# Kernel tuning notes

Hardware: AMD Instinct MI355X
Metric: run time of the kernel (lower is better)

The kernel has to match this reference:

```python
import jax, jax.numpy as jnp
import numpy as np

N = 50000      # nodes
E = 800000     # edges (avg degree 16)
DIN = 128      # input_dim
DG = 128       # gnn_dim
DCLS = 128     # cls_dim
DOUT = 10      # output_dim
LMDA = 1.0     # rw_lmda
P_DROP = 0.5


def setup_inputs() -> dict:
    key = jax.random.key(0)
    ks = jax.random.split(key, 12)
    x = jax.random.normal(ks[0], (N, DIN), jnp.float32)
    edge_index = jax.random.randint(ks[1], (2, E), 0, N, dtype=jnp.int64)
    edge_weight = jax.random.uniform(ks[2], (E,), jnp.float32)
    def glorot(k, shape):
        lim = np.sqrt(6.0 / (shape[0] + shape[1])).astype(np.float32)
        return jax.random.uniform(k, shape, jnp.float32, -lim, lim)
    return dict(
        x=x, edge_index=edge_index, edge_weight=edge_weight,
        W_lin_in=glorot(ks[3], (DIN, DG)), b_lin_in=jnp.zeros((DG,), jnp.float32),
        W_agg_in=glorot(ks[4], (DG + DIN, DG)), b_agg_in=jnp.zeros((DG,), jnp.float32),
        W_lin_h=glorot(ks[5], (DG, DG)), b_lin_h=jnp.zeros((DG,), jnp.float32),
        W_agg_h=glorot(ks[6], (2 * DG, DG)), b_agg_h=jnp.zeros((DG,), jnp.float32),
        W_mlp1=glorot(ks[7], (DG, DCLS)), b_mlp1=jnp.zeros((DCLS,), jnp.float32),
        W_mlp2=glorot(ks[8], (DCLS, DOUT)), b_mlp2=jnp.zeros((DOUT,), jnp.float32),
    )


def _gs_layer(x, row, col, ew, inv_cnt, W_lin, b_lin, W_agg, b_agg):
    # GS_reweight: message = (1-lmda)*lin(x_j) + lmda*ew*lin(x_j), mean-aggregated
    # at row (flow='target_to_source': gather from col, scatter to row).
    h = x @ W_lin + b_lin                      # [N, DG] (lin before gather == lin(x_j))
    hj = h[col]                                # [E, DG] gather
    m = (1.0 - LMDA) * hj + LMDA * (ew[:, None] * hj)
    agg = jax.ops.segment_sum(m, row, num_segments=N) * inv_cnt[:, None]  # mean
    out = jnp.concatenate([agg, x], axis=-1) @ W_agg + b_agg              # update()
    return jax.nn.relu(out)


def _dropout(x, k):
    mask = jax.random.bernoulli(k, 1.0 - P_DROP, x.shape)
    return jnp.where(mask, x / (1.0 - P_DROP), 0.0)


def reference(x, edge_index, edge_weight,
              W_lin_in, b_lin_in, W_agg_in, b_agg_in,
              W_lin_h, b_lin_h, W_agg_h, b_agg_h,
              W_mlp1, b_mlp1, W_mlp2, b_mlp2):
    row, col = edge_index[0], edge_index[1]
    cnt = jax.ops.segment_sum(jnp.ones((E,), x.dtype), row, num_segments=N)
    inv_cnt = 1.0 / jnp.maximum(cnt, 1.0)     # scatter_mean: empty rows -> 0
    dk = jax.random.split(jax.random.key(42), 3)
    h = _gs_layer(x, row, col, edge_weight, inv_cnt, W_lin_in, b_lin_in, W_agg_in, b_agg_in)
    h = _dropout(jax.nn.relu(h), dk[0])       # relu is idempotent after update's relu
    for i in range(2):                        # layers 2,3 share prop_hidden weights
        h = _gs_layer(h, row, col, edge_weight, inv_cnt, W_lin_h, b_lin_h, W_agg_h, b_agg_h)
        h = _dropout(jax.nn.relu(h), dk[i + 1])
    y = jax.nn.relu(h @ W_mlp1 + b_mlp1) @ W_mlp2 + b_mlp2  # cls_layers=2, bn=False
    return (h, y)
```

## Files before the change

kernel.cpp:

```cpp
#include <hip/hip_runtime.h>
#include <cstdint>
#include <cstddef>


#define N_NODES 50000
#define N_EDGES 800000
#define DGN 128
#define DOUT 10
#define NELEM (N_NODES * DGN)
#define NMASKW (NELEM / 64)
#define NBINS 391
#define TILE 4096
#define BSTR 4096
#define NTILES ((N_EDGES + TILE - 1) / TILE)
#define GB128 ((N_NODES + 127) / 128)
#define MK_BLOCKS 25000
#define MKB512 12500

#define XB_BLK 6250
#define HI_BLK NTILES
#define WC_BLK 128
#define TR_BLK 192
#define R0 XB_BLK
#define R1 (R0 + HI_BLK)
#define R2 (R1 + WC_BLK)
#define R3 (R2 + TR_BLK)
#define MEGA_BLOCKS (R3 + 1)

#define AB_BLOCKS ((N_NODES + 3) / 4)

typedef __attribute__((ext_vector_type(8))) short bf16x8;
typedef __attribute__((ext_vector_type(4))) float f32x4;

__host__ __device__ static inline unsigned short f2bf(float f) {
  union { float f; unsigned u; } c; c.f = f;
  unsigned u = c.u;
  return (unsigned short)((u + 0x7fffu + ((u >> 16) & 1u)) >> 16);
}
__device__ static inline float bflo(unsigned u) { return __uint_as_float(u << 16); }
__device__ static inline float bfhi(unsigned u) { return __uint_as_float(u & 0xffff0000u); }

__host__ __device__ static inline void tf2x32(unsigned k0, unsigned k1,
                                              unsigned c0, unsigned c1,
                                              unsigned& o0, unsigned& o1) {
  unsigned ks2 = k0 ^ k1 ^ 0x1BD11BDAu;
  unsigned x0 = c0 + k0;
  unsigned x1 = c1 + k1;
#define TFR(r) { x0 += x1; x1 = (x1 << (r)) | (x1 >> (32 - (r))); x1 ^= x0; }
  TFR(13) TFR(15) TFR(26) TFR(6)
  x0 += k1;  x1 += ks2 + 1u;
  TFR(17) TFR(29) TFR(16) TFR(24)
  x0 += ks2; x1 += k0 + 2u;
  TFR(13) TFR(15) TFR(26) TFR(6)
  x0 += k0;  x1 += k1 + 3u;
  TFR(17) TFR(29) TFR(16) TFR(24)
  x0 += k1;  x1 += ks2 + 4u;
  TFR(13) TFR(15) TFR(26) TFR(6)
  x0 += ks2; x1 += k0 + 5u;
#undef TFR
  o0 = x0; o1 = x1;
}

__device__ static inline void mask_chunk(unsigned long long* __restrict__ gm,
                                         int i, unsigned k0, unsigned k1) {
  unsigned o0, o1;
  tf2x32(k0, k1, 0u, (unsigned)i, o0, o1);
  unsigned long long b = __ballot(((o0 ^ o1) >> 31) == 0u);
  if ((threadIdx.x & 63) == 0) gm[i >> 6] = b;
}

__global__ __launch_bounds__(256) void mega_kernel(
    const float* __restrict__ x, unsigned short* __restrict__ xb,
    const int* __restrict__ ei, int* __restrict__ chist,
    const float* __restrict__ Wli, const float* __restrict__ Wai,
    const float* __restrict__ Wlh, const float* __restrict__ Wah,
    const float* __restrict__ Wm1,
    const float* __restrict__ bli, const float* __restrict__ blh,
    unsigned short* __restrict__ Tai, unsigned short* __restrict__ Tah,
    unsigned short* __restrict__ Tm1,
    float* __restrict__ bvi, float* __restrict__ bvh) {
  __shared__ int h[NBINS];
  const int b = blockIdx.x;
  const int tid = threadIdx.x;

  if (b < R0) {
    int g = b * 256 + tid;
    float4 v = ((const float4*)x)[g];
    ushort4 o;
    o.x = f2bf(v.x); o.y = f2bf(v.y); o.z = f2bf(v.z); o.w = f2bf(v.w);
    ((ushort4*)xb)[g] = o;
  } else if (b < R1) {
    for (int i = tid; i < NBINS; i += 256) h[i] = 0;
    __syncthreads();
    const int e0 = (b - R0) * TILE;
#pragma unroll 4
    for (int j = 0; j < TILE; j += 256) {
      int e = e0 + j + tid;
      if (e < N_EDGES) {
        int r = ei[e];
        r = (r < 0) ? 0 : (r >= N_NODES ? N_NODES - 1 : r);
        atomicAdd(&h[r >> 7], 1);
      }
    }
    __syncthreads();
    for (int i = tid; i < NBINS; i += 256)
      if (h[i]) atomicAdd(&chist[i], h[i]);
  } else if (b < R2) {
    int idx = (b - R1) * 256 + tid;
    int n = idx & 127;
    int k = (idx >> 7) & 127;
    int m = idx >> 14;
    const float* Wl = m ? Wlh : Wli;
    const float* Wa = m ? Wah : Wai;
    unsigned short* T = m ? Tah : Tai;
    float acc = 0.0f;
#pragma unroll 8
    for (int j = 0; j < 128; ++j)
      acc += Wl[k * 128 + j] * Wa[j * 128 + n];
    T[n * 256 + k] = f2bf(acc);
  } else if (b < R3) {
    int j = (b - R2) * 256 + tid;
    if (j < 16384) {
      int kk = j & 127, n = j >> 7;
      Tai[n * 256 + 128 + kk] = f2bf(Wai[(size_t)(128 + kk) * 128 + n]);
    } else if (j < 32768) {
      int q = j - 16384;
      int kk = q & 127, n = q >> 7;
      Tah[n * 256 + 128 + kk] = f2bf(Wah[(size_t)(128 + kk) * 128 + n]);
    } else {
      int q = j - 32768;
      int k = q & 127, n = q >> 7;
      Tm1[n * 128 + k] = f2bf(Wm1[(size_t)k * 128 + n]);
    }
  } else {
    int n = tid & 127;
    const float* bl = (tid < 128) ? bli : blh;
    const float* Wa = (tid < 128) ? Wai : Wah;
    float acc = 0.0f;
    for (int j = 0; j < 128; ++j) acc += bl[j] * Wa[j * 128 + n];
    if (tid < 128) bvi[n] = acc; else bvh[n] = acc;
  }
}

__global__ __launch_bounds__(256) void scatter_kernel(const int* __restrict__ ei,
                                                      const float* __restrict__ ew,
                                                      int* __restrict__ ccursor,
                                                      uint2* __restrict__ pk,
                                                      unsigned long long* __restrict__ mg0,
                                                      unsigned k00, unsigned k01) {
  if (blockIdx.x >= NTILES) {
    mask_chunk(mg0, (blockIdx.x - NTILES) * 256 + threadIdx.x, k00, k01);
    return;
  }
  __shared__ uint2 st[TILE];
  __shared__ unsigned short sbin[TILE];
  __shared__ int h[NBINS];
  __shared__ int base[NBINS];
  __shared__ int gbase[NBINS];
  __shared__ int cur[NBINS];
  __shared__ int sc[512];
  const int tid = threadIdx.x;
  const int e0 = blockIdx.x * TILE;
  const int nt = (N_EDGES - e0 < TILE) ? (N_EDGES - e0) : TILE;

  for (int i = tid; i < NBINS; i += 256) { h[i] = 0; cur[i] = 0; }
  __syncthreads();
  for (int j = tid; j < nt; j += 256) {
    int r = ei[e0 + j];
    r = (r < 0) ? 0 : (r >= N_NODES ? N_NODES - 1 : r);
    atomicAdd(&h[r >> 7], 1);
  }
  __syncthreads();
  sc[tid] = (tid < NBINS) ? h[tid] : 0;
  sc[tid + 256] = (tid + 256 < NBINS) ? h[tid + 256] : 0;
  __syncthreads();
  for (int off = 1; off < 512; off <<= 1) {
    int a0 = (tid >= off) ? sc[tid - off] : 0;
    int a1 = (tid + 256 >= off) ? sc[tid + 256 - off] : 0;
    __syncthreads();
    sc[tid] += a0; sc[tid + 256] += a1;
    __syncthreads();
  }
  if (tid < NBINS) {
    base[tid] = sc[tid] - h[tid];
    if (h[tid]) gbase[tid] = tid * BSTR + atomicAdd(&ccursor[tid], h[tid]);
  }
  if (tid + 256 < NBINS) {
    base[tid + 256] = sc[tid + 256] - h[tid + 256];
    if (h[tid + 256])
      gbase[tid + 256] = (tid + 256) * BSTR + atomicAdd(&ccursor[tid + 256], h[tid + 256]);
  }
  __syncthreads();
  for (int j = tid; j < nt; j += 256) {
    int r = ei[e0 + j];
    r = (r < 0) ? 0 : (r >= N_NODES ? N_NODES - 1 : r);
    int c = ei[N_EDGES + e0 + j];
    c = (c < 0) ? 0 : (c >= N_NODES ? N_NODES - 1 : c);
    int bb = r >> 7;
    int slot = base[bb] + atomicAdd(&cur[bb], 1);
    uint2 p;
    p.x = ((unsigned)r << 16) | (unsigned)c;
    p.y = __float_as_uint(ew[e0 + j]);
    st[slot] = p;
    sbin[slot] = (unsigned short)bb;
  }
  __syncthreads();
  for (int j = tid; j < nt; j += 256) {
    int bb = sbin[j];
    pk[(size_t)gbase[bb] + (j - base[bb])] = st[j];
  }
}

__global__ __launch_bounds__(256) void place_kernel(const int* __restrict__ chist,
                                                    const uint2* __restrict__ pk,
                                                    uint2* __restrict__ csr,
                                                    int* __restrict__ rowptr,
                                                    float* __restrict__ invc) {
  __shared__ int red[256];
  __shared__ int lcnt[128];
  __shared__ int lpre[128];
  __shared__ int lcur[128];
  __shared__ int sc[128];
  const int b = blockIdx.x;
  const int tid = threadIdx.x;

  int psum = 0;
  for (int i = tid; i < b; i += 256) psum += chist[i];
  red[tid] = psum;
  __syncthreads();
  for (int off = 128; off > 0; off >>= 1) {
    if (tid < off) red[tid] += red[tid + off];
    __syncthreads();
  }
  const int cb = red[0];
  const int n = chist[b];
  const uint2* __restrict__ pkb = pk + (size_t)b * BSTR;
  const int r0 = b << 7;
  const int nr = (N_NODES - r0 < 128) ? (N_NODES - r0) : 128;

  if (tid < 128) { lcnt[tid] = 0; lcur[tid] = 0; }
  __syncthreads();
  for (int i = tid; i < n; i += 256) {
    int r7 = (int)(pkb[i].x >> 16) - r0;
    atomicAdd(&lcnt[r7], 1);
  }
  __syncthreads();
  if (tid < 128) sc[tid] = lcnt[tid];
  __syncthreads();
  for (int off = 1; off < 128; off <<= 1) {
    int tv = (tid >= off && tid < 128) ? sc[tid - off] : 0;
    __syncthreads();
    if (tid < 128) sc[tid] += tv;
    __syncthreads();
  }
  if (tid < 128) lpre[tid] = sc[tid] - lcnt[tid];
  __syncthreads();
  if (tid < nr) {
    rowptr[r0 + tid] = cb + lpre[tid];
    int c = lcnt[tid];
    invc[r0 + tid] = 1.0f / (float)(c > 1 ? c : 1);
  }
  if (b == NBINS - 1 && tid == 0) rowptr[N_NODES] = N_EDGES;
  for (int i = tid; i < n; i += 256) {
    uint2 p = pkb[i];
    int r7 = (int)(p.x >> 16) - r0;
    int slot = cb + lpre[r7] + atomicAdd(&lcur[r7], 1);
    uint2 o;
    o.x = p.x & 0xFFFFu;
    o.y = p.y;
    csr[slot] = o;
  }
}

__global__ __launch_bounds__(256) void agg_kernel(const unsigned short* __restrict__ hlin,
                                                  const int* __restrict__ rowptr,
                                                  const uint2* __restrict__ csr,
                                                  const float* __restrict__ invc,
                                                  unsigned short* __restrict__ agg,
                                                  float* __restrict__ swout) {
  const int r = blockIdx.x * 4 + (threadIdx.x >> 6);
  const int lane = threadIdx.x & 63;
  const int es = lane >> 4;
  const int cg = lane & 15;
  const int start = rowptr[r];
  const int num = rowptr[r + 1] - start;
  const uint4* __restrict__ H = (const uint4*)hlin;

  int qi = (num > 0) ? (start + (lane < num ? lane : num - 1)) : 0;
  uint2 myq = csr[qi];

  float a[8] = {0.f, 0.f, 0.f, 0.f, 0.f, 0.f, 0.f, 0.f};
  float ws = 0.f;
  const int nb = (num < 64) ? num : 64;
  for (int e = 0; e < nb; e += 16) {
#pragma unroll
    for (int j = 0; j < 4; ++j) {
      int idx = e + j * 4 + es;
      bool ok = idx < nb;
      int sl = ok ? idx : nb - 1;
      int c0 = __shfl((int)myq.x, sl);
      int w0 = __shfl((int)myq.y, sl);
      unsigned col = (unsigned)c0;
      float w = ok ? __uint_as_float((unsigned)w0) : 0.0f;
      uint4 p = H[(size_t)col * 16 + cg];
      ws += w;
      a[0] += w * bflo(p.x); a[1] += w * bfhi(p.x);
      a[2] += w * bflo(p.y); a[3] += w * bfhi(p.y);
      a[4] += w * bflo(p.z); a[5] += w * bfhi(p.z);
      a[6] += w * bflo(p.w); a[7] += w * bfhi(p.w);
    }
  }
  for (int e = 64; e < num; e += 16) {
#pragma unroll
    for (int j = 0; j < 4; ++j) {
      int idx = e + j * 4 + es;
      bool ok = idx < num;
      int idxc = ok ? idx : (num - 1);
      uint2 q = csr[start + idxc];
      float w = ok ? __uint_as_float(q.y) : 0.0f;
      uint4 p = H[(size_t)q.x * 16 + cg];
      ws += w;
      a[0] += w * bflo(p.x); a[1] += w * bfhi(p.x);
      a[2] += w * bflo(p.y); a[3] += w * bfhi(p.y);
      a[4] += w * bflo(p.z); a[5] += w * bfhi(p.z);
      a[6] += w * bflo(p.w); a[7] += w * bfhi(p.w);
    }
  }
#pragma unroll
  for (int k = 0; k < 8; ++k) {
    a[k] += __shfl_xor(a[k], 32);
    a[k] += __shfl_xor(a[k], 16);
  }
  ws += __shfl_xor(ws, 32);
  ws += __shfl_xor(ws, 16);
  const float s = invc[r];
  if (es == 0) {
    uint4 o;
    o.x = (unsigned)f2bf(a[0] * s) | ((unsigned)f2bf(a[1] * s) << 16);
    o.y = (unsigned)f2bf(a[2] * s) | ((unsigned)f2bf(a[3] * s) << 16);
    o.z = (unsigned)f2bf(a[4] * s) | ((unsigned)f2bf(a[5] * s) << 16);
    o.w = (unsigned)f2bf(a[6] * s) | ((unsigned)f2bf(a[7] * s) << 16);
    ((uint4*)agg)[(size_t)r * 16 + cg] = o;
  }
  if (swout && lane == 0) swout[r] = ws * s;
}

template <bool WF32, bool MASKGEN, bool MLP>
__global__ __launch_bounds__(512) void layer_gemm(
    const unsigned short* __restrict__ Agg, const unsigned short* __restrict__ Hin,
    const unsigned short* __restrict__ Wt,
    const float* __restrict__ bvec, const float* __restrict__ bagg,
    const float* __restrict__ sw,
    const unsigned long long* __restrict__ maskw,
    float* __restrict__ outf, unsigned short* __restrict__ outb,
    unsigned long long* __restrict__ gm, unsigned gk0, unsigned gk1,
    const unsigned short* __restrict__ Wt2,
    const float* __restrict__ b1,
    const float* __restrict__ W2, const float* __restrict__ b2,
    float* __restrict__ y) {
  if (MASKGEN && blockIdx.x >= GB128) {
    mask_chunk(gm, (blockIdx.x - GB128) * 512 + threadIdx.x, gk0, gk1);
    return;
  }
  constexpr int LS = 72;
  constexpr int LT = 132;
  __shared__ unsigned short Als[128 * LS];
  __shared__ unsigned short Bls[128 * LS];
  __shared__ unsigned short tT[MLP ? 128 * LT : 2];
  __shared__ unsigned short Wsb[MLP ? 16 * LT : 2];
  __shared__ float bs[MLP ? DOUT : 1];
  const int tid = threadIdx.x;
  const int m0 = blockIdx.x * 128;
  const int lane = tid & 63;
  const int wid = tid >> 6;
  const int wm = (wid >> 1) * 32;
  const int wn = (wid & 1) * 64;
  const int ln = lane & 15;
  const int lh = lane >> 4;
  const int sArow = tid >> 2;
  const int sAk = (tid & 3) * 16;
  int arow = m0 + sArow;
  if (arow >= N_NODES) arow = N_NODES - 1;

  if (MLP) {
    for (int i = tid; i < 16 * 128; i += 512) {
      int c = i >> 7, k = i & 127;
      Wsb[c * LT + k] = (c < DOUT) ? f2bf(W2[(size_t)k * DOUT + c]) : (unsigned short)0;
    }
    if (tid < DOUT) bs[tid] = b2[tid];
  }

  f32x4 acc[2][4];
#pragma unroll
  for (int i = 0; i < 2; ++i)
#pragma unroll
    for (int j = 0; j < 4; ++j)
#pragma unroll
      for (int r = 0; r < 4; ++r) acc[i][j][r] = 0.0f;

  for (int kb = 0; kb < 256; kb += 64) {
    const unsigned short* Asrc = (kb < 128) ? Agg : Hin;
    const unsigned short* ap = Asrc + (size_t)arow * 128 + (kb & 127) + sAk;
    unsigned short* al = &Als[sArow * LS + sAk];
    *(uint4*)(al + 0) = *(const uint4*)(ap + 0);
    *(uint4*)(al + 8) = *(const uint4*)(ap + 8);
    const unsigned short* bp = Wt + (size_t)sArow * 256 + kb + sAk;
    unsigned short* bl = &Bls[sArow * LS + sAk];
    *(uint4*)(bl + 0) = *(const uint4*)(bp + 0);
    *(uint4*)(bl + 8) = *(const uint4*)(bp + 8);
    __syncthreads();
#pragma unroll
    for (int ks = 0; ks < 64; ks += 32) {
      bf16x8 af[2], bfr[4];
#pragma unroll
      for (int i = 0; i < 2; ++i)
        af[i] = *(const bf16x8*)&Als[(wm + i * 16 + ln) * LS + ks + lh * 8];
#pragma unroll
      for (int j = 0; j < 4; ++j)
        bfr[j] = *(const bf16x8*)&Bls[(wn + j * 16 + ln) * LS + ks + lh * 8];
#pragma unroll
      for (int i = 0; i < 2; ++i)
#pragma unroll
        for (int j = 0; j < 4; ++j)
          acc[i][j] = __builtin_amdgcn_mfma_f32_16x16x32_bf16(af[i], bfr[j], acc[i][j], 0, 0, 0);
    }
    __syncthreads();
  }

  const int lm = lane >> 4;
  float bc[4], b2c[4];
#pragma unroll
  for (int j = 0; j < 4; ++j) {
    int col = wn + j * 16 + ln;
    bc[j] = bvec[col];
    b2c[j] = bagg[col];
  }
#pragma unroll
  for (int i = 0; i < 2; ++i) {
    const int lr0 = wm + i * 16 + lm * 4;
#pragma unroll
    for (int r = 0; r < 4; ++r) {
      const int row = m0 + lr0 + r;
      if (row >= N_NODES) continue;
      const float swr = sw[row];
      const unsigned long long mw = maskw[(size_t)row * 2 + (wn >> 6)];
#pragma unroll
      for (int j = 0; j < 4; ++j) {
        const int col = wn + j * 16 + ln;
        float v = acc[i][j][r] + swr * bc[j] + b2c[j];
        v = fmaxf(v, 0.0f);
        v = ((mw >> (col & 63)) & 1ull) ? 2.0f * v : 0.0f;
        if (WF32) outf[(size_t)row * DGN + col] = v;
        if (MLP) tT[(lr0 + r) * LT + col] = f2bf(v);
        else outb[(size_t)row * DGN + col] = f2bf(v);
      }
    }
  }

  if (MLP) {
    __syncthreads();

    f32x4 acc2[2][4];
#pragma unroll
    for (int i = 0; i < 2; ++i)
#pragma unroll
      for (int j = 0; j < 4; ++j)
#pragma unroll
        for (int r = 0; r < 4; ++r) acc2[i][j][r] = 0.0f;

    for (int kb = 0; kb < 128; kb += 64) {
      const unsigned short* bp = Wt2 + (size_t)sArow * 128 + kb + sAk;
      unsigned short* bl = &Bls[sArow * LS + sAk];
      *(uint4*)(bl + 0) = *(const uint4*)(bp + 0);
      *(uint4*)(bl + 8) = *(const uint4*)(bp + 8);
      __syncthreads();
#pragma unroll
      for (int ks = 0; ks < 64; ks += 32) {
        bf16x8 af[2], bfr[4];
#pragma unroll
        for (int i = 0; i < 2; ++i)
          af[i] = *(const bf16x8*)&tT[(wm + i * 16 + ln) * LT + kb + ks + lh * 8];
#pragma unroll
        for (int j = 0; j < 4; ++j)
          bfr[j] = *(const bf16x8*)&Bls[(wn + j * 16 + ln) * LS + ks + lh * 8];
#pragma unroll
        for (int i = 0; i < 2; ++i)
#pragma unroll
          for (int j = 0; j < 4; ++j)
            acc2[i][j] = __builtin_amdgcn_mfma_f32_16x16x32_bf16(af[i], bfr[j], acc2[i][j], 0, 0, 0);
      }
      __syncthreads();
    }

    float bcol[4];
#pragma unroll
    for (int j = 0; j < 4; ++j) bcol[j] = b1[wn + j * 16 + ln];
#pragma unroll
    for (int i = 0; i < 2; ++i) {
      const int lr0 = wm + i * 16 + lm * 4;
#pragma unroll
      for (int r = 0; r < 4; ++r) {
        const int lr = lr0 + r;
#pragma unroll
        for (int j = 0; j < 4; ++j) {
          const int col = wn + j * 16 + ln;
          float v = fmaxf(acc2[i][j][r] + bcol[j], 0.0f);
          tT[lr * LT + col] = f2bf(v);
        }
      }
    }
    __syncthreads();

    f32x4 acc3;
#pragma unroll
    for (int r = 0; r < 4; ++r) acc3[r] = 0.0f;
#pragma unroll
    for (int kt = 0; kt < 4; ++kt) {
      bf16x8 af = *(const bf16x8*)&tT[(wid * 16 + ln) * LT + kt * 32 + lh * 8];
      bf16x8 bw = *(const bf16x8*)&Wsb[ln * LT + kt * 32 + lh * 8];
      acc3 = __builtin_amdgcn_mfma_f32_16x16x32_bf16(af, bw, acc3, 0, 0, 0);
    }
    if (ln < DOUT) {
#pragma unroll
      for (int r = 0; r < 4; ++r) {
        const int row = m0 + wid * 16 + lm * 4 + r;
        if (row < N_NODES) y[(size_t)row * DOUT + ln] = acc3[r] + bs[ln];
      }
    }
  }
}

extern "C" void kernel_launch(void* const* d_in, const int* in_sizes, int n_in,
                              void* d_out, int out_size, void* d_ws, size_t ws_size,
                              hipStream_t stream) {
  const float* x        = (const float*)d_in[0];
  const int*   ei       = (const int*)d_in[1];
  const float* ew       = (const float*)d_in[2];
  const float* W_lin_in = (const float*)d_in[3];
  const float* b_lin_in = (const float*)d_in[4];
  const float* W_agg_in = (const float*)d_in[5];
  const float* b_agg_in = (const float*)d_in[6];
  const float* W_lin_h  = (const float*)d_in[7];
  const float* b_lin_h  = (const float*)d_in[8];
  const float* W_agg_h  = (const float*)d_in[9];
  const float* b_agg_h  = (const float*)d_in[10];
  const float* W_mlp1   = (const float*)d_in[11];
  const float* b_mlp1   = (const float*)d_in[12];
  const float* W_mlp2   = (const float*)d_in[13];
  const float* b_mlp2   = (const float*)d_in[14];

  float* hout = (float*)d_out;
  float* yout = hout + (size_t)NELEM;

  char* p = (char*)d_ws;
  auto alloc = [&](size_t bytes) {
    char* q = p;
    p += (bytes + 255) & ~(size_t)255;
    return q;
  };
  int*   chist   = (int*)alloc((size_t)(NBINS + 1) * 4);
  int*   ccursor = (int*)alloc((size_t)NBINS * 4);
  int*   rowptr  = (int*)alloc((size_t)(N_NODES + 1) * 4);
  float* invc    = (float*)alloc((size_t)N_NODES * 4);
  float* swv     = (float*)alloc((size_t)N_NODES * 4);
  uint2* pk      = (uint2*)alloc((size_t)NBINS * BSTR * 8);
  uint2* csr     = (uint2*)alloc((size_t)N_EDGES * 8);
  unsigned short* xb   = (unsigned short*)alloc((size_t)NELEM * 2);
  unsigned short* aggb = (unsigned short*)alloc((size_t)NELEM * 2);
  unsigned short* hA   = (unsigned short*)alloc((size_t)NELEM * 2);
  unsigned short* hB   = (unsigned short*)alloc((size_t)NELEM * 2);
  unsigned long long* mw0 = (unsigned long long*)alloc((size_t)NMASKW * 8);
  unsigned long long* mw1 = (unsigned long long*)alloc((size_t)NMASKW * 8);
  unsigned long long* mw2 = (unsigned long long*)alloc((size_t)NMASKW * 8);
  unsigned short* Tai = (unsigned short*)alloc(32768 * 2);
  unsigned short* Tah = (unsigned short*)alloc(32768 * 2);
  unsigned short* Tm1 = (unsigned short*)alloc(16384 * 2);
  float* bvi = (float*)alloc(128 * 4);
  float* bvh = (float*)alloc(128 * 4);

  unsigned dk[3][2];
  for (unsigned i = 0; i < 3; ++i) tf2x32(0u, 42u, 0u, i, dk[i][0], dk[i][1]);

  hipMemsetAsync(chist, 0, (size_t)(NBINS + 1) * 4, stream);
  hipMemsetAsync(ccursor, 0, (size_t)NBINS * 4, stream);
  mega_kernel<<<MEGA_BLOCKS, 256, 0, stream>>>(
      x, xb, ei, chist, W_lin_in, W_agg_in, W_lin_h, W_agg_h, W_mlp1,
      b_lin_in, b_lin_h, Tai, Tah, Tm1, bvi, bvh);

  scatter_kernel<<<NTILES + MK_BLOCKS, 256, 0, stream>>>(
      ei, ew, ccursor, pk, mw0, dk[0][0], dk[0][1]);
  place_kernel<<<NBINS, 256, 0, stream>>>(chist, pk, csr, rowptr, invc);

  agg_kernel<<<AB_BLOCKS, 256, 0, stream>>>(xb, rowptr, csr, invc, aggb, swv);
  layer_gemm<false, true, false><<<GB128 + MKB512, 512, 0, stream>>>(
      aggb, xb, Tai, bvi, b_agg_in, swv, mw0, nullptr, hA,
      mw1, dk[1][0], dk[1][1], nullptr, nullptr, nullptr, nullptr, nullptr);

  agg_kernel<<<AB_BLOCKS, 256, 0, stream>>>(hA, rowptr, csr, invc, aggb, nullptr);
  layer_gemm<false, true, false><<<GB128 + MKB512, 512, 0, stream>>>(
      aggb, hA, Tah, bvh, b_agg_h, swv, mw1, nullptr, hB,
      mw2, dk[2][0], dk[2][1], nullptr, nullptr, nullptr, nullptr, nullptr);

  agg_kernel<<<AB_BLOCKS, 256, 0, stream>>>(hB, rowptr, csr, invc, aggb, nullptr);
  layer_gemm<true, false, true><<<GB128, 512, 0, stream>>>(
      aggb, hB, Tah, bvh, b_agg_h, swv, mw2, hout, nullptr,
      nullptr, 0, 0, Tm1, b_mlp1, W_mlp2, b_mlp2, yout);
}
```

Before: 295.8 us.

## Fuse neighbor aggregation into the per-layer GEMM kernel via shared memory

Removes the standalone agg_kernel. Each 128-row GEMM block now gathers and mean-aggregates its own rows' neighbor features into an LDS tile (AggT), along with the per-row weight sums. The first half of the K loop reads A from that LDS tile instead of global memory. This drops the global aggregate buffer, its write and read traffic, and three kernel launches. In exchange the latency-bound gather runs inside far fewer, larger blocks (one wave walks 16 rows sequentially) with more LDS per block, so there is less parallelism to hide gather latency.

```diff
diff --git a/kernel.cpp b/kernel.cpp
--- a/kernel.cpp
+++ b/kernel.cpp
@@ -26,8 +26,6 @@
 #define R2 (R1 + WC_BLK)
 #define R3 (R2 + TR_BLK)
 #define MEGA_BLOCKS (R3 + 1)
-
-#define AB_BLOCKS ((N_NODES + 3) / 4)
 
 typedef __attribute__((ext_vector_type(8))) short bf16x8;
 typedef __attribute__((ext_vector_type(4))) float f32x4;
@@ -272,85 +270,14 @@
   }
 }
 
-__global__ __launch_bounds__(256) void agg_kernel(const unsigned short* __restrict__ hlin,
-                                                  const int* __restrict__ rowptr,
-                                                  const uint2* __restrict__ csr,
-                                                  const float* __restrict__ invc,
-                                                  unsigned short* __restrict__ agg,
-                                                  float* __restrict__ swout) {
-  const int r = blockIdx.x * 4 + (threadIdx.x >> 6);
-  const int lane = threadIdx.x & 63;
-  const int es = lane >> 4;
-  const int cg = lane & 15;
-  const int start = rowptr[r];
-  const int num = rowptr[r + 1] - start;
-  const uint4* __restrict__ H = (const uint4*)hlin;
-
-  int qi = (num > 0) ? (start + (lane < num ? lane : num - 1)) : 0;
-  uint2 myq = csr[qi];
-
-  float a[8] = {0.f, 0.f, 0.f, 0.f, 0.f, 0.f, 0.f, 0.f};
-  float ws = 0.f;
-  const int nb = (num < 64) ? num : 64;
-  for (int e = 0; e < nb; e += 16) {
-#pragma unroll
-    for (int j = 0; j < 4; ++j) {
-      int idx = e + j * 4 + es;
-      bool ok = idx < nb;
-      int sl = ok ? idx : nb - 1;
-      int c0 = __shfl((int)myq.x, sl);
-      int w0 = __shfl((int)myq.y, sl);
-      unsigned col = (unsigned)c0;
-      float w = ok ? __uint_as_float((unsigned)w0) : 0.0f;
-      uint4 p = H[(size_t)col * 16 + cg];
-      ws += w;
-      a[0] += w * bflo(p.x); a[1] += w * bfhi(p.x);
-      a[2] += w * bflo(p.y); a[3] += w * bfhi(p.y);
-      a[4] += w * bflo(p.z); a[5] += w * bfhi(p.z);
-      a[6] += w * bflo(p.w); a[7] += w * bfhi(p.w);
-    }
-  }
-  for (int e = 64; e < num; e += 16) {
-#pragma unroll
-    for (int j = 0; j < 4; ++j) {
-      int idx = e + j * 4 + es;
-      bool ok = idx < num;
-      int idxc = ok ? idx : (num - 1);
-      uint2 q = csr[start + idxc];
-      float w = ok ? __uint_as_float(q.y) : 0.0f;
-      uint4 p = H[(size_t)q.x * 16 + cg];
-      ws += w;
-      a[0] += w * bflo(p.x); a[1] += w * bfhi(p.x);
-      a[2] += w * bflo(p.y); a[3] += w * bfhi(p.y);
-      a[4] += w * bflo(p.z); a[5] += w * bfhi(p.z);
-      a[6] += w * bflo(p.w); a[7] += w * bfhi(p.w);
-    }
-  }
-#pragma unroll
-  for (int k = 0; k < 8; ++k) {
-    a[k] += __shfl_xor(a[k], 32);
-    a[k] += __shfl_xor(a[k], 16);
-  }
-  ws += __shfl_xor(ws, 32);
-  ws += __shfl_xor(ws, 16);
-  const float s = invc[r];
-  if (es == 0) {
-    uint4 o;
-    o.x = (unsigned)f2bf(a[0] * s) | ((unsigned)f2bf(a[1] * s) << 16);
-    o.y = (unsigned)f2bf(a[2] * s) | ((unsigned)f2bf(a[3] * s) << 16);
-    o.z = (unsigned)f2bf(a[4] * s) | ((unsigned)f2bf(a[5] * s) << 16);
-    o.w = (unsigned)f2bf(a[6] * s) | ((unsigned)f2bf(a[7] * s) << 16);
-    ((uint4*)agg)[(size_t)r * 16 + cg] = o;
-  }
-  if (swout && lane == 0) swout[r] = ws * s;
-}
-
 template <bool WF32, bool MASKGEN, bool MLP>
-__global__ __launch_bounds__(512) void layer_gemm(
-    const unsigned short* __restrict__ Agg, const unsigned short* __restrict__ Hin,
+__global__ __launch_bounds__(512) void layer_fused(
+    const unsigned short* __restrict__ Hin,
+    const int* __restrict__ rowptr,
+    const uint2* __restrict__ csr,
+    const float* __restrict__ invc,
     const unsigned short* __restrict__ Wt,
     const float* __restrict__ bvec, const float* __restrict__ bagg,
-    const float* __restrict__ sw,
     const unsigned long long* __restrict__ maskw,
     float* __restrict__ outf, unsigned short* __restrict__ outb,
     unsigned long long* __restrict__ gm, unsigned gk0, unsigned gk1,
@@ -363,12 +290,13 @@
     return;
   }
   constexpr int LS = 72;
-  constexpr int LT = 132;
+  constexpr int LT = 136;
+  __shared__ unsigned short AggT[128 * LT];
   __shared__ unsigned short Als[128 * LS];
   __shared__ unsigned short Bls[128 * LS];
-  __shared__ unsigned short tT[MLP ? 128 * LT : 2];
   __shared__ unsigned short Wsb[MLP ? 16 * LT : 2];
   __shared__ float bs[MLP ? DOUT : 1];
+  __shared__ float sws[128];
   const int tid = threadIdx.x;
   const int m0 = blockIdx.x * 128;
   const int lane = tid & 63;
@@ -390,6 +318,74 @@
     if (tid < DOUT) bs[tid] = b2[tid];
   }
 
+  {
+    const uint4* __restrict__ H = (const uint4*)Hin;
+    const int es = lane >> 4;
+    const int cg = lane & 15;
+    for (int t = 0; t < 16; ++t) {
+      const int rl = wid * 16 + t;
+      const int r = m0 + rl;
+      int start = 0, num = 0;
+      if (r < N_NODES) { start = rowptr[r]; num = rowptr[r + 1] - start; }
+      int qi = (num > 0) ? (start + (lane < num ? lane : num - 1)) : 0;
+      uint2 myq = csr[qi];
+      float a[8] = {0.f, 0.f, 0.f, 0.f, 0.f, 0.f, 0.f, 0.f};
+      float ws = 0.f;
+      const int nbv = (num < 64) ? num : 64;
+      for (int e = 0; e < nbv; e += 16) {
+#pragma unroll
+        for (int j = 0; j < 4; ++j) {
+          int idx = e + j * 4 + es;
+          bool ok = idx < nbv;
+          int sl = ok ? idx : nbv - 1;
+          int c0 = __shfl((int)myq.x, sl);
+          int w0 = __shfl((int)myq.y, sl);
+          unsigned col = (unsigned)c0;
+          float w = ok ? __uint_as_float((unsigned)w0) : 0.0f;
+          uint4 p = H[(size_t)col * 16 + cg];
+          ws += w;
+          a[0] += w * bflo(p.x); a[1] += w * bfhi(p.x);
+          a[2] += w * bflo(p.y); a[3] += w * bfhi(p.y);
+          a[4] += w * bflo(p.z); a[5] += w * bfhi(p.z);
+          a[6] += w * bflo(p.w); a[7] += w * bfhi(p.w);
+        }
+      }
+      for (int e = 64; e < num; e += 16) {
+#pragma unroll
+        for (int j = 0; j < 4; ++j) {
+          int idx = e + j * 4 + es;
+          bool ok = idx < num;
+          int idxc = ok ? idx : (num - 1);
+          uint2 q = csr[start + idxc];
+          float w = ok ? __uint_as_float(q.y) : 0.0f;
+          uint4 p = H[(size_t)q.x * 16 + cg];
+          ws += w;
+          a[0] += w * bflo(p.x); a[1] += w * bfhi(p.x);
+          a[2] += w * bflo(p.y); a[3] += w * bfhi(p.y);
+          a[4] += w * bflo(p.z); a[5] += w * bfhi(p.z);
+          a[6] += w * bflo(p.w); a[7] += w * bfhi(p.w);
+        }
+      }
+#pragma unroll
+      for (int k = 0; k < 8; ++k) {
+        a[k] += __shfl_xor(a[k], 32);
+        a[k] += __shfl_xor(a[k], 16);
+      }
+      ws += __shfl_xor(ws, 32);
+      ws += __shfl_xor(ws, 16);
+      const float s = (r < N_NODES) ? invc[r] : 0.0f;
+      if (es == 0) {
+        uint4 o;
+        o.x = (unsigned)f2bf(a[0] * s) | ((unsigned)f2bf(a[1] * s) << 16);
+        o.y = (unsigned)f2bf(a[2] * s) | ((unsigned)f2bf(a[3] * s) << 16);
+        o.z = (unsigned)f2bf(a[4] * s) | ((unsigned)f2bf(a[5] * s) << 16);
+        o.w = (unsigned)f2bf(a[6] * s) | ((unsigned)f2bf(a[7] * s) << 16);
+        *(uint4*)&AggT[rl * LT + cg * 8] = o;
+      }
+      if (lane == 0) sws[rl] = ws * s;
+    }
+  }
+
   f32x4 acc[2][4];
 #pragma unroll
   for (int i = 0; i < 2; ++i)
@@ -399,11 +395,12 @@
       for (int r = 0; r < 4; ++r) acc[i][j][r] = 0.0f;
 
   for (int kb = 0; kb < 256; kb += 64) {
-    const unsigned short* Asrc = (kb < 128) ? Agg : Hin;
-    const unsigned short* ap = Asrc + (size_t)arow * 128 + (kb & 127) + sAk;
-    unsigned short* al = &Als[sArow * LS + sAk];
-    *(uint4*)(al + 0) = *(const uint4*)(ap + 0);
-    *(uint4*)(al + 8) = *(const uint4*)(ap + 8);
+    if (kb >= 128) {
+      const unsigned short* ap = Hin + (size_t)arow * 128 + (kb & 127) + sAk;
+      unsigned short* al = &Als[sArow * LS + sAk];
+      *(uint4*)(al + 0) = *(const uint4*)(ap + 0);
+      *(uint4*)(al + 8) = *(const uint4*)(ap + 8);
+    }
     const unsigned short* bp = Wt + (size_t)sArow * 256 + kb + sAk;
     unsigned short* bl = &Bls[sArow * LS + sAk];
     *(uint4*)(bl + 0) = *(const uint4*)(bp + 0);
@@ -414,7 +411,9 @@
       bf16x8 af[2], bfr[4];
 #pragma unroll
       for (int i = 0; i < 2; ++i)
-        af[i] = *(const bf16x8*)&Als[(wm + i * 16 + ln) * LS + ks + lh * 8];
+        af[i] = (kb < 128)
+            ? *(const bf16x8*)&AggT[(wm + i * 16 + ln) * LT + kb + ks + lh * 8]
+            : *(const bf16x8*)&Als[(wm + i * 16 + ln) * LS + ks + lh * 8];
 #pragma unroll
       for (int j = 0; j < 4; ++j)
         bfr[j] = *(const bf16x8*)&Bls[(wn + j * 16 + ln) * LS + ks + lh * 8];
@@ -442,7 +441,7 @@
     for (int r = 0; r < 4; ++r) {
       const int row = m0 + lr0 + r;
       if (row >= N_NODES) continue;
-      const float swr = sw[row];
+      const float swr = sws[lr0 + r];
       const unsigned long long mw = maskw[(size_t)row * 2 + (wn >> 6)];
 #pragma unroll
       for (int j = 0; j < 4; ++j) {
@@ -451,7 +450,7 @@
         v = fmaxf(v, 0.0f);
         v = ((mw >> (col & 63)) & 1ull) ? 2.0f * v : 0.0f;
         if (WF32) outf[(size_t)row * DGN + col] = v;
-        if (MLP) tT[(lr0 + r) * LT + col] = f2bf(v);
+        if (MLP) AggT[(lr0 + r) * LT + col] = f2bf(v);
         else outb[(size_t)row * DGN + col] = f2bf(v);
       }
     }
@@ -479,7 +478,7 @@
         bf16x8 af[2], bfr[4];
 #pragma unroll
         for (int i = 0; i < 2; ++i)
-          af[i] = *(const bf16x8*)&tT[(wm + i * 16 + ln) * LT + kb + ks + lh * 8];
+          af[i] = *(const bf16x8*)&AggT[(wm + i * 16 + ln) * LT + kb + ks + lh * 8];
 #pragma unroll
         for (int j = 0; j < 4; ++j)
           bfr[j] = *(const bf16x8*)&Bls[(wn + j * 16 + ln) * LS + ks + lh * 8];
@@ -505,7 +504,7 @@
         for (int j = 0; j < 4; ++j) {
           const int col = wn + j * 16 + ln;
           float v = fmaxf(acc2[i][j][r] + bcol[j], 0.0f);
-          tT[lr * LT + col] = f2bf(v);
+          AggT[lr * LT + col] = f2bf(v);
         }
       }
     }
@@ -516,7 +515,7 @@
     for (int r = 0; r < 4; ++r) acc3[r] = 0.0f;
 #pragma unroll
     for (int kt = 0; kt < 4; ++kt) {
-      bf16x8 af = *(const bf16x8*)&tT[(wid * 16 + ln) * LT + kt * 32 + lh * 8];
+      bf16x8 af = *(const bf16x8*)&AggT[(wid * 16 + ln) * LT + kt * 32 + lh * 8];
       bf16x8 bw = *(const bf16x8*)&Wsb[ln * LT + kt * 32 + lh * 8];
       acc3 = __builtin_amdgcn_mfma_f32_16x16x32_bf16(af, bw, acc3, 0, 0, 0);
     }
@@ -562,11 +561,9 @@
   int*   ccursor = (int*)alloc((size_t)NBINS * 4);
   int*   rowptr  = (int*)alloc((size_t)(N_NODES + 1) * 4);
   float* invc    = (float*)alloc((size_t)N_NODES * 4);
-  float* swv     = (float*)alloc((size_t)N_NODES * 4);
   uint2* pk      = (uint2*)alloc((size_t)NBINS * BSTR * 8);
   uint2* csr     = (uint2*)alloc((size_t)N_EDGES * 8);
   unsigned short* xb   = (unsigned short*)alloc((size_t)NELEM * 2);
-  unsigned short* aggb = (unsigned short*)alloc((size_t)NELEM * 2);
   unsigned short* hA   = (unsigned short*)alloc((size_t)NELEM * 2);
   unsigned short* hB   = (unsigned short*)alloc((size_t)NELEM * 2);
   unsigned long long* mw0 = (unsigned long long*)alloc((size_t)NMASKW * 8);
@@ -591,18 +588,15 @@
       ei, ew, ccursor, pk, mw0, dk[0][0], dk[0][1]);
   place_kernel<<<NBINS, 256, 0, stream>>>(chist, pk, csr, rowptr, invc);
 
-  agg_kernel<<<AB_BLOCKS, 256, 0, stream>>>(xb, rowptr, csr, invc, aggb, swv);
-  layer_gemm<false, true, false><<<GB128 + MKB512, 512, 0, stream>>>(
-      aggb, xb, Tai, bvi, b_agg_in, swv, mw0, nullptr, hA,
+  layer_fused<false, true, false><<<GB128 + MKB512, 512, 0, stream>>>(
+      xb, rowptr, csr, invc, Tai, bvi, b_agg_in, mw0, nullptr, hA,
       mw1, dk[1][0], dk[1][1], nullptr, nullptr, nullptr, nullptr, nullptr);
 
-  agg_kernel<<<AB_BLOCKS, 256, 0, stream>>>(hA, rowptr, csr, invc, aggb, nullptr);
-  layer_gemm<false, true, false><<<GB128 + MKB512, 512, 0, stream>>>(
-      aggb, hA, Tah, bvh, b_agg_h, swv, mw1, nullptr, hB,
+  layer_fused<false, true, false><<<GB128 + MKB512, 512, 0, stream>>>(
+      hA, rowptr, csr, invc, Tah, bvh, b_agg_h, mw1, nullptr, hB,
       mw2, dk[2][0], dk[2][1], nullptr, nullptr, nullptr, nullptr, nullptr);
 
-  agg_kernel<<<AB_BLOCKS, 256, 0, stream>>>(hB, rowptr, csr, invc, aggb, nullptr);
-  layer_gemm<true, false, true><<<GB128, 512, 0, stream>>>(
-      aggb, hB, Tah, bvh, b_agg_h, swv, mw2, hout, nullptr,
+  layer_fused<true, false, true><<<GB128, 512, 0, stream>>>(
+      hB, rowptr, csr, invc, Tah, bvh, b_agg_h, mw2, hout, nullptr,
       nullptr, 0, 0, Tm1, b_mlp1, W_mlp2, b_mlp2, yout);
 }
```

Result: slower. 311.4 us (+5.3%).
